# Optimization experiments

Measured on AMD Instinct MI355X. Metric: run time of the kernel, lower is better.

Reference implementation:

```python
import jax, jax.numpy as jnp
import numpy as np

R = 1.1
SCALE = 100.0
BUMP_STEPS = 32
NUM_THETAS = 32
NUM_FEATURES = 128
N_NODES = 200000
NUM_GRAPHS = 128


def setup_inputs() -> dict:
    key = jax.random.key(0)
    k1, k2, k3 = jax.random.split(key, 3)
    x = jax.random.normal(k1, (N_NODES, NUM_FEATURES), dtype=jnp.float32)
    batch = jnp.sort(jax.random.randint(k2, (N_NODES,), 0, NUM_GRAPHS, dtype=jnp.int64))
    v = jax.random.uniform(k3, (NUM_THETAS, NUM_FEATURES), dtype=jnp.float32) - 0.5
    return {"x": x, "batch": batch, "num_graphs": NUM_GRAPHS, "v": v}


def reference(x, batch, num_graphs, v):
    # nh: node heights along each direction theta -> [N, T]
    nh = x @ v.T
    # linspace over filtration values -> [S]
    lin = jnp.linspace(-R, R, BUMP_STEPS, dtype=nh.dtype)
    # bump: sigmoid difference; second point is the constant pad value R
    # ecc: [N, S, T]  (node-major so segment_sum reduces the leading axis)
    ecc = (jax.nn.sigmoid(SCALE * (lin[None, :, None] - nh[:, None, :]))
           - jax.nn.sigmoid(SCALE * (lin - R))[None, :, None])
    # scatter-add per graph label -> [ng, S, T] == index_add over dim1 then movedim(0,1)
    ect = jax.ops.segment_sum(ecc, batch, num_segments=num_graphs)
    return ect
```

## Files before the change

kernel.cpp:

```cpp
#include <hip/hip_runtime.h>
#include <math.h>

#define N_NODES 200000
#define NF 128
#define NT 32
#define NS 32
#define NG 128
#define ATILE 64
#define ABLOCKS 3125
#define HPAD 33

typedef short bf16x8 __attribute__((ext_vector_type(8)));
typedef float floatx4 __attribute__((ext_vector_type(4)));

__device__ __forceinline__ float rcp_fast(float x) { return __builtin_amdgcn_rcpf(x); }

__device__ __forceinline__ void split_bf16(float f, unsigned short& h, unsigned short& l) {
    unsigned u  = __float_as_uint(f);
    unsigned r  = u + 0x7FFFu + ((u >> 16) & 1u);
    unsigned hb = r & 0xFFFF0000u;
    h = (unsigned short)(hb >> 16);
    float rem = f - __uint_as_float(hb);
    unsigned u2 = __float_as_uint(rem);
    unsigned r2 = u2 + 0x7FFFu + ((u2 >> 16) & 1u);
    l = (unsigned short)(r2 >> 16);
}

__device__ __forceinline__ void split8(float4 a, float4 b, bf16x8& h8, bf16x8& l8) {
    unsigned short h[8], l[8];
    split_bf16(a.x, h[0], l[0]); split_bf16(a.y, h[1], l[1]);
    split_bf16(a.z, h[2], l[2]); split_bf16(a.w, h[3], l[3]);
    split_bf16(b.x, h[4], l[4]); split_bf16(b.y, h[5], l[5]);
    split_bf16(b.z, h[6], l[6]); split_bf16(b.w, h[7], l[7]);
    h8 = (bf16x8){(short)h[0],(short)h[1],(short)h[2],(short)h[3],
                  (short)h[4],(short)h[5],(short)h[6],(short)h[7]};
    l8 = (bf16x8){(short)l[0],(short)l[1],(short)l[2],(short)l[3],
                  (short)l[4],(short)l[5],(short)l[6],(short)l[7]};
}

__global__ __launch_bounds__(256)
void prep_v(const float* __restrict__ v,
            unsigned short* __restrict__ vh,
            unsigned short* __restrict__ vl)
{
    int j = blockIdx.x * 256 + threadIdx.x;
    if (j >= NT * NF / 4) return;
    float4 val = ((const float4*)v)[j];
    unsigned short h0,h1,h2,h3,l0,l1,l2,l3;
    split_bf16(val.x, h0, l0); split_bf16(val.y, h1, l1);
    split_bf16(val.z, h2, l2); split_bf16(val.w, h3, l3);
    ((ushort4*)vh)[j] = make_ushort4(h0, h1, h2, h3);
    ((ushort4*)vl)[j] = make_ushort4(l0, l1, l2, l3);
}

__global__ __launch_bounds__(256, 6)
void ect_fused(const float* __restrict__ x,
               const int* __restrict__ batch,
               const unsigned short* __restrict__ vh,
               const unsigned short* __restrict__ vl,
               float* __restrict__ out)
{
    __shared__ unsigned hist[NT * HPAD];
    __shared__ float    corr[NT * HPAD];
    __shared__ float    cnt_lds;

    const int tid  = threadIdx.x;
    const int blk  = blockIdx.x;
    const int w    = tid >> 6;
    const int lane = tid & 63;
    const int mrow = lane & 15;
    const int quad = lane >> 4;

    const size_t arow = (size_t)blk * ATILE + w * 16 + mrow;
    const float* __restrict__ xrow = x + arow * NF + quad * 8;

    bf16x8 ah[4], al[4];
    #pragma unroll
    for (int slice = 0; slice < 4; ++slice) {
        float4 a0 = *(const float4*)&xrow[slice * 32];
        float4 a1 = *(const float4*)&xrow[slice * 32 + 4];
        split8(a0, a1, ah[slice], al[slice]);
    }

    floatx4 acc0 = {0.f, 0.f, 0.f, 0.f};
    floatx4 acc1 = {0.f, 0.f, 0.f, 0.f};
    const int b0off = mrow * NF + quad * 8;
    const int b1off = (16 + mrow) * NF + quad * 8;
    #pragma unroll
    for (int slice = 0; slice < 4; ++slice) {
        bf16x8 bh0 = *(const bf16x8*)&vh[b0off + slice * 32];
        bf16x8 bl0 = *(const bf16x8*)&vl[b0off + slice * 32];
        bf16x8 bh1 = *(const bf16x8*)&vh[b1off + slice * 32];
        bf16x8 bl1 = *(const bf16x8*)&vl[b1off + slice * 32];
        acc0 = __builtin_amdgcn_mfma_f32_16x16x32_bf16(ah[slice], bh0, acc0, 0, 0, 0);
        acc0 = __builtin_amdgcn_mfma_f32_16x16x32_bf16(ah[slice], bl0, acc0, 0, 0, 0);
        acc0 = __builtin_amdgcn_mfma_f32_16x16x32_bf16(al[slice], bh0, acc0, 0, 0, 0);
        acc1 = __builtin_amdgcn_mfma_f32_16x16x32_bf16(ah[slice], bh1, acc1, 0, 0, 0);
        acc1 = __builtin_amdgcn_mfma_f32_16x16x32_bf16(ah[slice], bl1, acc1, 0, 0, 0);
        acc1 = __builtin_amdgcn_mfma_f32_16x16x32_bf16(al[slice], bh1, acc1, 0, 0, 0);
    }

    const int base = blk * ATILE;
    const int g_first = batch[base];
    const int g_last  = batch[base + ATILE - 1];
    int nlabel[4];
    #pragma unroll
    for (int reg = 0; reg < 4; ++reg)
        nlabel[reg] = batch[base + w * 16 + quad * 4 + reg];

    const float inv_dlin = 14.090909090909092f;
    const float Lw       = 10.23848093f;
    const float dlin     = 2.2f / 31.0f;
    const float L        = 144.26950408889634f;

    const int ft = tid & 31;
    const int sb = tid >> 5;

    for (int gp = g_first; gp <= g_last; ++gp) {
        for (int i = tid; i < NT * HPAD; i += 256) { hist[i] = 0u; corr[i] = 0.0f; }
        __syncthreads();

        #pragma unroll
        for (int reg = 0; reg < 4; ++reg) {
            if (nlabel[reg] == gp) {
                #pragma unroll
                for (int half = 0; half < 2; ++half) {
                    int   t = half ? (16 + mrow) : mrow;
                    float h = half ? acc1[reg] : acc0[reg];
                    float z = fmaf(h, inv_dlin, 15.5f);
                    int s_up = (int)ceilf(z);
                    s_up = min(max(s_up, 0), 32);
                    atomicAdd(&hist[t * HPAD + s_up], 1u);
                    int s0 = (int)ceilf(z - 1.45f);
                    #pragma unroll
                    for (int i2 = 0; i2 < 3; ++i2) {
                        int s = s0 + i2;
                        float e   = __builtin_amdgcn_exp2f(Lw * (z - (float)s));
                        float sig = rcp_fast(1.0f + e);
                        float stp = (s >= s_up) ? 1.0f : 0.0f;
                        if (s >= 0 && s <= 31) atomicAdd(&corr[t * HPAD + s], sig - stp);
                    }
                }
            }
        }
        __syncthreads();

        if (tid < ATILE) {
            unsigned long long m = __ballot(batch[base + tid] == gp);
            if (tid == 0) cnt_lds = (float)__popcll(m);
        }
        {
            const int grp = tid >> 5;
            const int s   = tid & 31;
            for (int row = grp; row < NT; row += 8) {
                float val = (float)hist[row * HPAD + s];
                #pragma unroll
                for (int d = 1; d < 32; d <<= 1) {
                    float nbr = __shfl_up(val, d, 32);
                    if (s >= d) val += nbr;
                }
                corr[row * HPAD + s] += val;
            }
        }
        __syncthreads();

        #pragma unroll
        for (int k = 0; k < 4; ++k) {
            int s = sb + 8 * k;
            float lin_s = -1.1f + (float)s * dlin;
            float cs  = rcp_fast(1.0f + __builtin_amdgcn_exp2f(L * (1.1f - lin_s)));
            float val = corr[ft * HPAD + s] - cnt_lds * cs;
            atomicAdd(&out[(size_t)gp * (NS * NT) + s * NT + ft], val);
        }
        if (gp < g_last) __syncthreads();
    }
}

extern "C" void kernel_launch(void* const* d_in, const int* in_sizes, int n_in,
                              void* d_out, int out_size, void* d_ws, size_t ws_size,
                              hipStream_t stream) {
    const float* x     = (const float*)d_in[0];
    const int*   batch = (const int*)d_in[1];
    const float* v     = (const float*)d_in[3];
    float*       out   = (float*)d_out;

    unsigned short* vh = (unsigned short*)d_ws;
    unsigned short* vl = vh + NT * NF;

    hipMemsetAsync(d_out, 0, (size_t)out_size * sizeof(float), stream);
    prep_v<<<dim3(4), dim3(256), 0, stream>>>(v, vh, vl);
    ect_fused<<<dim3(ABLOCKS), dim3(256), 0, stream>>>(x, batch, vh, vl, out);
}
```

Measured before the change: 170.8 us.

## Process four node tiles per block and flush histograms only on graph change

Each block now walks four consecutive 64-node tiles and keeps its shared-memory histogram and correction accumulators across tiles. It writes them to global memory with atomics only when the graph label changes or at the end. Because batch is sorted, this cuts the number of global atomic flushes and the per-tile LDS zeroing and sync overhead by about four times. The cost is fewer blocks (782), lower occupancy bounds and serial tile processing within a block, which may reduce latency hiding.

```diff
diff --git a/kernel.cpp b/kernel.cpp
--- a/kernel.cpp
+++ b/kernel.cpp
@@ -6,8 +6,9 @@
 #define NT 32
 #define NS 32
 #define NG 128
-#define ATILE 64
-#define ABLOCKS 3125
+#define BTILE 4
+#define BNODES 256
+#define NBLOCKS 782
 #define HPAD 33
 
 typedef short bf16x8 __attribute__((ext_vector_type(8)));
@@ -53,7 +54,7 @@
     ((ushort4*)vl)[j] = make_ushort4(l0, l1, l2, l3);
 }
 
-__global__ __launch_bounds__(256, 6)
+__global__ __launch_bounds__(256, 4)
 void ect_fused(const float* __restrict__ x,
                const int* __restrict__ batch,
                const unsigned short* __restrict__ vh,
@@ -62,7 +63,7 @@
 {
     __shared__ unsigned hist[NT * HPAD];
     __shared__ float    corr[NT * HPAD];
-    __shared__ float    cnt_lds;
+    __shared__ float    cntw[4];
 
     const int tid  = threadIdx.x;
     const int blk  = blockIdx.x;
@@ -71,42 +72,21 @@
     const int mrow = lane & 15;
     const int quad = lane >> 4;
 
-    const size_t arow = (size_t)blk * ATILE + w * 16 + mrow;
-    const float* __restrict__ xrow = x + arow * NF + quad * 8;
-
-    bf16x8 ah[4], al[4];
-    #pragma unroll
-    for (int slice = 0; slice < 4; ++slice) {
-        float4 a0 = *(const float4*)&xrow[slice * 32];
-        float4 a1 = *(const float4*)&xrow[slice * 32 + 4];
-        split8(a0, a1, ah[slice], al[slice]);
-    }
-
-    floatx4 acc0 = {0.f, 0.f, 0.f, 0.f};
-    floatx4 acc1 = {0.f, 0.f, 0.f, 0.f};
+    const int base   = blk * BNODES;
+    const int nnodes = min(BNODES, N_NODES - base);
+    const int ntiles = nnodes >> 6;
+
+    const int  myidx   = base + tid;
+    const int  mylabel = batch[(myidx < N_NODES) ? myidx : (N_NODES - 1)];
+    const bool cvalid  = (tid < nnodes);
+
+    int gp = batch[base];
+
+    for (int i = tid; i < NT * HPAD; i += 256) { hist[i] = 0u; corr[i] = 0.0f; }
+    __syncthreads();
+
     const int b0off = mrow * NF + quad * 8;
     const int b1off = (16 + mrow) * NF + quad * 8;
-    #pragma unroll
-    for (int slice = 0; slice < 4; ++slice) {
-        bf16x8 bh0 = *(const bf16x8*)&vh[b0off + slice * 32];
-        bf16x8 bl0 = *(const bf16x8*)&vl[b0off + slice * 32];
-        bf16x8 bh1 = *(const bf16x8*)&vh[b1off + slice * 32];
-        bf16x8 bl1 = *(const bf16x8*)&vl[b1off + slice * 32];
-        acc0 = __builtin_amdgcn_mfma_f32_16x16x32_bf16(ah[slice], bh0, acc0, 0, 0, 0);
-        acc0 = __builtin_amdgcn_mfma_f32_16x16x32_bf16(ah[slice], bl0, acc0, 0, 0, 0);
-        acc0 = __builtin_amdgcn_mfma_f32_16x16x32_bf16(al[slice], bh0, acc0, 0, 0, 0);
-        acc1 = __builtin_amdgcn_mfma_f32_16x16x32_bf16(ah[slice], bh1, acc1, 0, 0, 0);
-        acc1 = __builtin_amdgcn_mfma_f32_16x16x32_bf16(ah[slice], bl1, acc1, 0, 0, 0);
-        acc1 = __builtin_amdgcn_mfma_f32_16x16x32_bf16(al[slice], bh1, acc1, 0, 0, 0);
-    }
-
-    const int base = blk * ATILE;
-    const int g_first = batch[base];
-    const int g_last  = batch[base + ATILE - 1];
-    int nlabel[4];
-    #pragma unroll
-    for (int reg = 0; reg < 4; ++reg)
-        nlabel[reg] = batch[base + w * 16 + quad * 4 + reg];
 
     const float inv_dlin = 14.090909090909092f;
     const float Lw       = 10.23848093f;
@@ -116,63 +96,129 @@
     const int ft = tid & 31;
     const int sb = tid >> 5;
 
-    for (int gp = g_first; gp <= g_last; ++gp) {
-        for (int i = tid; i < NT * HPAD; i += 256) { hist[i] = 0u; corr[i] = 0.0f; }
-        __syncthreads();
-
+    for (int tile = 0; tile < ntiles; ++tile) {
+        const int trow = base + tile * 64;
+
+        const float* __restrict__ xrow = x + (size_t)(trow + w * 16 + mrow) * NF + quad * 8;
+        bf16x8 ah[4], al[4];
         #pragma unroll
-        for (int reg = 0; reg < 4; ++reg) {
-            if (nlabel[reg] == gp) {
-                #pragma unroll
-                for (int half = 0; half < 2; ++half) {
-                    int   t = half ? (16 + mrow) : mrow;
-                    float h = half ? acc1[reg] : acc0[reg];
-                    float z = fmaf(h, inv_dlin, 15.5f);
-                    int s_up = (int)ceilf(z);
-                    s_up = min(max(s_up, 0), 32);
-                    atomicAdd(&hist[t * HPAD + s_up], 1u);
-                    int s0 = (int)ceilf(z - 1.45f);
+        for (int s = 0; s < 4; ++s) {
+            float4 a0 = *(const float4*)&xrow[s * 32];
+            float4 a1 = *(const float4*)&xrow[s * 32 + 4];
+            split8(a0, a1, ah[s], al[s]);
+        }
+
+        floatx4 acc0 = {0.f, 0.f, 0.f, 0.f};
+        floatx4 acc1 = {0.f, 0.f, 0.f, 0.f};
+        #pragma unroll
+        for (int s = 0; s < 4; ++s) {
+            bf16x8 bh0 = *(const bf16x8*)&vh[b0off + s * 32];
+            bf16x8 bl0 = *(const bf16x8*)&vl[b0off + s * 32];
+            bf16x8 bh1 = *(const bf16x8*)&vh[b1off + s * 32];
+            bf16x8 bl1 = *(const bf16x8*)&vl[b1off + s * 32];
+            acc0 = __builtin_amdgcn_mfma_f32_16x16x32_bf16(ah[s], bh0, acc0, 0, 0, 0);
+            acc0 = __builtin_amdgcn_mfma_f32_16x16x32_bf16(ah[s], bl0, acc0, 0, 0, 0);
+            acc0 = __builtin_amdgcn_mfma_f32_16x16x32_bf16(al[s], bh0, acc0, 0, 0, 0);
+            acc1 = __builtin_amdgcn_mfma_f32_16x16x32_bf16(ah[s], bh1, acc1, 0, 0, 0);
+            acc1 = __builtin_amdgcn_mfma_f32_16x16x32_bf16(ah[s], bl1, acc1, 0, 0, 0);
+            acc1 = __builtin_amdgcn_mfma_f32_16x16x32_bf16(al[s], bh1, acc1, 0, 0, 0);
+        }
+
+        int nlabel[4];
+        #pragma unroll
+        for (int reg = 0; reg < 4; ++reg)
+            nlabel[reg] = batch[trow + w * 16 + quad * 4 + reg];
+        const int tlast = batch[trow + 63];
+
+        while (true) {
+            #pragma unroll
+            for (int reg = 0; reg < 4; ++reg) {
+                if (nlabel[reg] == gp) {
                     #pragma unroll
-                    for (int i2 = 0; i2 < 3; ++i2) {
-                        int s = s0 + i2;
-                        float e   = __builtin_amdgcn_exp2f(Lw * (z - (float)s));
-                        float sig = rcp_fast(1.0f + e);
-                        float stp = (s >= s_up) ? 1.0f : 0.0f;
-                        if (s >= 0 && s <= 31) atomicAdd(&corr[t * HPAD + s], sig - stp);
+                    for (int half = 0; half < 2; ++half) {
+                        int   t = half ? (16 + mrow) : mrow;
+                        float h = half ? acc1[reg] : acc0[reg];
+                        float z = fmaf(h, inv_dlin, 15.5f);
+                        int s_up = (int)ceilf(z);
+                        s_up = min(max(s_up, 0), 32);
+                        atomicAdd(&hist[t * HPAD + s_up], 1u);
+                        int s0 = (int)ceilf(z - 1.45f);
+                        #pragma unroll
+                        for (int i2 = 0; i2 < 3; ++i2) {
+                            int s = s0 + i2;
+                            float e   = __builtin_amdgcn_exp2f(Lw * (z - (float)s));
+                            float sig = rcp_fast(1.0f + e);
+                            float stp = (s >= s_up) ? 1.0f : 0.0f;
+                            if (s >= 0 && s <= 31) atomicAdd(&corr[t * HPAD + s], sig - stp);
+                        }
                     }
                 }
             }
-        }
-        __syncthreads();
-
-        if (tid < ATILE) {
-            unsigned long long m = __ballot(batch[base + tid] == gp);
-            if (tid == 0) cnt_lds = (float)__popcll(m);
-        }
-        {
-            const int grp = tid >> 5;
-            const int s   = tid & 31;
-            for (int row = grp; row < NT; row += 8) {
-                float val = (float)hist[row * HPAD + s];
-                #pragma unroll
-                for (int d = 1; d < 32; d <<= 1) {
-                    float nbr = __shfl_up(val, d, 32);
-                    if (s >= d) val += nbr;
+            if (tlast <= gp) break;
+
+            __syncthreads();
+            {
+                unsigned long long m = __ballot(cvalid && (mylabel == gp));
+                if (lane == 0) cntw[w] = (float)__popcll(m);
+            }
+            {
+                const int grp = tid >> 5;
+                const int s   = tid & 31;
+                for (int row = grp; row < NT; row += 8) {
+                    float val = (float)hist[row * HPAD + s];
+                    #pragma unroll
+                    for (int d = 1; d < 32; d <<= 1) {
+                        float nbr = __shfl_up(val, d, 32);
+                        if (s >= d) val += nbr;
+                    }
+                    corr[row * HPAD + s] += val;
                 }
-                corr[row * HPAD + s] += val;
-            }
-        }
-        __syncthreads();
-
-        #pragma unroll
-        for (int k = 0; k < 4; ++k) {
-            int s = sb + 8 * k;
-            float lin_s = -1.1f + (float)s * dlin;
-            float cs  = rcp_fast(1.0f + __builtin_amdgcn_exp2f(L * (1.1f - lin_s)));
-            float val = corr[ft * HPAD + s] - cnt_lds * cs;
-            atomicAdd(&out[(size_t)gp * (NS * NT) + s * NT + ft], val);
-        }
-        if (gp < g_last) __syncthreads();
+            }
+            __syncthreads();
+            float cnt = cntw[0] + cntw[1] + cntw[2] + cntw[3];
+            #pragma unroll
+            for (int k = 0; k < 4; ++k) {
+                int s = sb + 8 * k;
+                float lin_s = -1.1f + (float)s * dlin;
+                float cs  = rcp_fast(1.0f + __builtin_amdgcn_exp2f(L * (1.1f - lin_s)));
+                float val = corr[ft * HPAD + s] - cnt * cs;
+                atomicAdd(&out[(size_t)gp * (NS * NT) + s * NT + ft], val);
+                corr[ft * HPAD + s] = 0.0f;
+                hist[ft * HPAD + s] = 0u;
+            }
+            if (sb == 0) { hist[ft * HPAD + 32] = 0u; corr[ft * HPAD + 32] = 0.0f; }
+            __syncthreads();
+            ++gp;
+        }
+    }
+
+    __syncthreads();
+    {
+        unsigned long long m = __ballot(cvalid && (mylabel == gp));
+        if (lane == 0) cntw[w] = (float)__popcll(m);
+    }
+    {
+        const int grp = tid >> 5;
+        const int s   = tid & 31;
+        for (int row = grp; row < NT; row += 8) {
+            float val = (float)hist[row * HPAD + s];
+            #pragma unroll
+            for (int d = 1; d < 32; d <<= 1) {
+                float nbr = __shfl_up(val, d, 32);
+                if (s >= d) val += nbr;
+            }
+            corr[row * HPAD + s] += val;
+        }
+    }
+    __syncthreads();
+    float cnt = cntw[0] + cntw[1] + cntw[2] + cntw[3];
+    #pragma unroll
+    for (int k = 0; k < 4; ++k) {
+        int s = sb + 8 * k;
+        float lin_s = -1.1f + (float)s * dlin;
+        float cs  = rcp_fast(1.0f + __builtin_amdgcn_exp2f(L * (1.1f - lin_s)));
+        float val = corr[ft * HPAD + s] - cnt * cs;
+        atomicAdd(&out[(size_t)gp * (NS * NT) + s * NT + ft], val);
     }
 }
 
@@ -189,5 +235,5 @@
 
     hipMemsetAsync(d_out, 0, (size_t)out_size * sizeof(float), stream);
     prep_v<<<dim3(4), dim3(256), 0, stream>>>(v, vh, vl);
-    ect_fused<<<dim3(ABLOCKS), dim3(256), 0, stream>>>(x, batch, vh, vl, out);
-}
+    ect_fused<<<dim3(NBLOCKS), dim3(256), 0, stream>>>(x, batch, vh, vl, out);
+}
```

Measured after the change: 194.0 us. 13.6% more time.
